# Kernel tuning notes

Hardware: AMD Instinct MI355X
Metric: run time of the kernel (lower is better)

Reference implementation:

```python
import jax, jax.numpy as jnp
import numpy as np

DIM = 512
EPS = 1e-08
N_LAYERS = 3


def setup_inputs() -> dict:
    key = jax.random.key(0)
    ks = jax.random.split(key, 1 + 2 * N_LAYERS)
    B, N1 = 4, 2049  # batch, tokens (1 cls + 2048 feat)
    x = jax.random.normal(ks[0], (B, N1, DIM), dtype=jnp.float32)
    inp = {"x": x}
    s = 1.0 / np.sqrt(DIM)
    for i in range(N_LAYERS):
        inp[f"W{i}"] = jax.random.uniform(ks[1 + 2 * i], (DIM, DIM), jnp.float32, -s, s)
        inp[f"b{i}"] = jax.random.uniform(ks[2 + 2 * i], (DIM,), jnp.float32, -s, s)
    return inp


def _pgcn(x, Ws, bs):
    cls_token = x[:, 0]          # [B, D]
    feat = x[:, 1:]              # [B, N, D]
    n = jnp.linalg.norm(feat, axis=2, keepdims=True)
    feat_norm = feat / jnp.maximum(n, EPS)
    sim = jnp.einsum('bnd,bmd->bnm', feat_norm, feat_norm)  # [B, N, N]
    N = sim.shape[1]
    topk = max(int(N * 0.01), 100)
    # torch.topk(largest=False): kth-smallest value per row is the threshold
    kth_smallest = -jax.lax.top_k(-sim, topk)[0][..., -1:]  # [B, N, 1]
    adj = jnp.where(sim >= kth_smallest, sim, 0.0)
    # 3-layer GCN (skip_connection=False, eval mode -> dropout is identity)
    h = feat
    for W, b in zip(Ws, bs):
        support = jnp.einsum('bnd,de->bne', h, W) + b
        h = jax.nn.relu(jnp.einsum('bnm,bmd->bnd', adj, support))
    return jnp.concatenate([cls_token[:, None, :], h], axis=1)


def reference(x, W0, b0, W1, b1, W2, b2):
    return _pgcn(x, (W0, W1, W2), (b0, b1, b2))
```

## Files before the change

kernel.cpp:

```cpp
#include <hip/hip_runtime.h>
#include <hip/hip_bf16.h>
#include <math.h>

#define DIMV   512
#define NTOK   2048
#define NROWS  2049
#define NB     4
#define KSEL   100
#define EPSV   1e-8f

typedef __bf16 bf16x8 __attribute__((ext_vector_type(8)));
typedef float  f32x4  __attribute__((ext_vector_type(4)));

__device__ __forceinline__ unsigned short f2bf(float f) {
  unsigned int u = __float_as_uint(f);
  u += 0x7fffu + ((u >> 16) & 1u);
  return (unsigned short)(u >> 16);
}
__device__ __forceinline__ float bf2f(unsigned short s) {
  return __uint_as_float(((unsigned int)s) << 16);
}

#define GLDS16(g, l)                                                         \
  __builtin_amdgcn_global_load_lds(                                          \
      (const __attribute__((address_space(1))) void*)(unsigned long long)(g),\
      (__attribute__((address_space(3))) void*)(unsigned int)(unsigned long long)(l), \
      16, 0, 0)

__global__ __launch_bounds__(256) void normalize_kernel(const float* __restrict__ x,
                                                        unsigned short* __restrict__ fhi,
                                                        unsigned short* __restrict__ flo,
                                                        unsigned short* __restrict__ featb) {
  const int wave = blockIdx.x * 4 + (threadIdx.x >> 6);
  const int lane = threadIdx.x & 63;
  const int b = wave / NTOK, r = wave % NTOK;
  const float* src = x + (long)(b * NROWS + 1 + r) * DIMV;
  const long rowoff = (long)(b * NTOK + r) * DIMV;
  float4 v0 = reinterpret_cast<const float4*>(src)[lane];
  float4 v1 = reinterpret_cast<const float4*>(src)[lane + 64];
  ushort4 u0, u1;
  u0.x = f2bf(v0.x); u0.y = f2bf(v0.y); u0.z = f2bf(v0.z); u0.w = f2bf(v0.w);
  u1.x = f2bf(v1.x); u1.y = f2bf(v1.y); u1.z = f2bf(v1.z); u1.w = f2bf(v1.w);
  reinterpret_cast<ushort4*>(featb + rowoff)[lane] = u0;
  reinterpret_cast<ushort4*>(featb + rowoff)[lane + 64] = u1;
  float ss = v0.x*v0.x + v0.y*v0.y + v0.z*v0.z + v0.w*v0.w
           + v1.x*v1.x + v1.y*v1.y + v1.z*v1.z + v1.w*v1.w;
  #pragma unroll
  for (int m = 1; m < 64; m <<= 1) ss += __shfl_xor(ss, m, 64);
  const float scale = 1.0f / fmaxf(sqrtf(ss), EPSV);
  float f[8] = {v0.x*scale, v0.y*scale, v0.z*scale, v0.w*scale,
                v1.x*scale, v1.y*scale, v1.z*scale, v1.w*scale};
  ushort4 h0, h1, l0, l1;
  unsigned short hh[8], ll[8];
  #pragma unroll
  for (int i = 0; i < 8; i++) {
    hh[i] = f2bf(f[i]);
    ll[i] = f2bf(f[i] - bf2f(hh[i]));
  }
  h0.x = hh[0]; h0.y = hh[1]; h0.z = hh[2]; h0.w = hh[3];
  h1.x = hh[4]; h1.y = hh[5]; h1.z = hh[6]; h1.w = hh[7];
  l0.x = ll[0]; l0.y = ll[1]; l0.z = ll[2]; l0.w = ll[3];
  l1.x = ll[4]; l1.y = ll[5]; l1.z = ll[6]; l1.w = ll[7];
  reinterpret_cast<ushort4*>(fhi + rowoff)[lane]      = h0;
  reinterpret_cast<ushort4*>(fhi + rowoff)[lane + 64] = h1;
  reinterpret_cast<ushort4*>(flo + rowoff)[lane]      = l0;
  reinterpret_cast<ushort4*>(flo + rowoff)[lane + 64] = l1;
}

__global__ __launch_bounds__(256) void prep_kernel(const float* __restrict__ W0,
                                                   const float* __restrict__ W1,
                                                   const float* __restrict__ W2,
                                                   unsigned short* __restrict__ WT,
                                                   const float* __restrict__ x,
                                                   float* __restrict__ out) {
  const int z = blockIdx.z;
  if (z == 3) {
    if (blockIdx.y == 0 && blockIdx.x < 8) {
      const int b = blockIdx.x >> 1, half = blockIdx.x & 1;
      const long off = (long)b * NROWS * DIMV + half * 256 + threadIdx.x;
      out[off] = x[off];
    }
    return;
  }
  const float* W = (z == 0) ? W0 : (z == 1) ? W1 : W2;
  unsigned short* WTl = WT + (long)z * DIMV * DIMV;
  __shared__ float tile[32][33];
  const int tx = threadIdx.x & 31, ty = threadIdx.x >> 5;
  const int bx = blockIdx.x, by = blockIdx.y;
  #pragma unroll
  for (int s = 0; s < 32; s += 8)
    tile[ty + s][tx] = W[(long)(by * 32 + ty + s) * DIMV + bx * 32 + tx];
  __syncthreads();
  #pragma unroll
  for (int s = 0; s < 32; s += 8)
    WTl[(long)(bx * 32 + ty + s) * DIMV + by * 32 + tx] = f2bf(tile[tx][ty + s]);
}

__global__ __launch_bounds__(256)
void sim_split_kernel(const unsigned short* __restrict__ Fhi,
                      const unsigned short* __restrict__ Flo,
                      float* __restrict__ C)
{
  __shared__ unsigned short AsH[128 * 32];
  __shared__ unsigned short AsL[128 * 32];
  __shared__ unsigned short BsH[128 * 32];
  __shared__ unsigned short BsL[128 * 32];
  const int t = threadIdx.x;
  const int l = t & 63;
  const int w = t >> 6;
  const int wr = w >> 1, wc = w & 1;
  const int zb = blockIdx.z;
  const int ti = blockIdx.x;
  int by = (int)((sqrtf(8.0f * (float)ti + 1.0f) - 1.0f) * 0.5f);
  while ((by + 1) * (by + 2) / 2 <= ti) by++;
  while (by * (by + 1) / 2 > ti) by--;
  const int bx = ti - by * (by + 1) / 2;
  const unsigned short* Ahi = Fhi + (long)zb * NTOK * DIMV;
  const unsigned short* Alo = Flo + (long)zb * NTOK * DIMV;
  const int row0 = by * 128;
  const int col0 = bx * 128;

  f32x4 acc[4][4];
  #pragma unroll
  for (int m = 0; m < 4; m++)
    #pragma unroll
    for (int n = 0; n < 4; n++) acc[m][n] = (f32x4){0.f, 0.f, 0.f, 0.f};

  const int r0 = t >> 2;
  const int r1 = 64 + (t >> 2);
  const int part = t & 3;
  const size_t base0 = (size_t)((t & 192) * 8);
  const size_t base1 = (size_t)((256 + (t & 192)) * 8);
  const int fr = l & 15, fg = l >> 4;

  for (int k0 = 0; k0 < DIMV; k0 += 32) {
    GLDS16(Ahi + (long)(row0 + r0) * DIMV + k0 + part * 8, AsH + base0);
    GLDS16(Ahi + (long)(row0 + r1) * DIMV + k0 + part * 8, AsH + base1);
    GLDS16(Alo + (long)(row0 + r0) * DIMV + k0 + part * 8, AsL + base0);
    GLDS16(Alo + (long)(row0 + r1) * DIMV + k0 + part * 8, AsL + base1);
    GLDS16(Ahi + (long)(col0 + r0) * DIMV + k0 + part * 8, BsH + base0);
    GLDS16(Ahi + (long)(col0 + r1) * DIMV + k0 + part * 8, BsH + base1);
    GLDS16(Alo + (long)(col0 + r0) * DIMV + k0 + part * 8, BsL + base0);
    GLDS16(Alo + (long)(col0 + r1) * DIMV + k0 + part * 8, BsL + base1);
    __syncthreads();

    bf16x8 ah[4], al[4], bh[4], bl[4];
    #pragma unroll
    for (int m = 0; m < 4; m++) {
      const int off = (wr * 64 + m * 16 + fr) * 32 + fg * 8;
      ah[m] = *reinterpret_cast<const bf16x8*>(&AsH[off]);
      al[m] = *reinterpret_cast<const bf16x8*>(&AsL[off]);
    }
    #pragma unroll
    for (int n = 0; n < 4; n++) {
      const int off = (wc * 64 + n * 16 + fr) * 32 + fg * 8;
      bh[n] = *reinterpret_cast<const bf16x8*>(&BsH[off]);
      bl[n] = *reinterpret_cast<const bf16x8*>(&BsL[off]);
    }
    #pragma unroll
    for (int m = 0; m < 4; m++)
      #pragma unroll
      for (int n = 0; n < 4; n++) {
        acc[m][n] = __builtin_amdgcn_mfma_f32_16x16x32_bf16(ah[m], bh[n], acc[m][n], 0, 0, 0);
        acc[m][n] = __builtin_amdgcn_mfma_f32_16x16x32_bf16(ah[m], bl[n], acc[m][n], 0, 0, 0);
        acc[m][n] = __builtin_amdgcn_mfma_f32_16x16x32_bf16(al[m], bh[n], acc[m][n], 0, 0, 0);
      }
    __syncthreads();
  }

  float* Cb = C + (long)zb * NTOK * NTOK;
  #pragma unroll
  for (int m = 0; m < 4; m++)
    #pragma unroll
    for (int r = 0; r < 4; r++) {
      const int row = row0 + wr * 64 + m * 16 + fg * 4 + r;
      #pragma unroll
      for (int n = 0; n < 4; n++) {
        const int col = col0 + wc * 64 + n * 16 + fr;
        Cb[(long)row * NTOK + col] = acc[m][n][r];
      }
    }
  if (bx != by) {
    #pragma unroll
    for (int m = 0; m < 4; m++)
      #pragma unroll
      for (int r = 0; r < 4; r++) {
        const int row = row0 + wr * 64 + m * 16 + fg * 4 + r;
        #pragma unroll
        for (int n = 0; n < 4; n++) {
          const int col = col0 + wc * 64 + n * 16 + fr;
          Cb[(long)col * NTOK + row] = acc[m][n][r];
        }
      }
  }
}

template<bool BIAS, bool RELU, bool BF16OUT>
__device__ __forceinline__
void gemm_body(const unsigned short* __restrict__ A,
               const unsigned short* __restrict__ Bt,
               const float* __restrict__ bias,
               void* __restrict__ Cv,
               int K, int lda, int ldb, int ldc,
               long sA, long sB, long sC,
               int bx, int by, int bz,
               unsigned short* As, unsigned short* Bs)
{
  const int t = threadIdx.x;
  const int l = t & 63;
  const int w = t >> 6;
  const int wr = w >> 1, wc = w & 1;
  A  += (long)bz * sA;
  Bt += (long)bz * sB;
  const int row0 = by * 128;
  const int col0 = bx * 64;

  f32x4 acc[4][2];
  #pragma unroll
  for (int m = 0; m < 4; m++)
    #pragma unroll
    for (int n = 0; n < 2; n++) acc[m][n] = (f32x4){0.f, 0.f, 0.f, 0.f};

  const int arow0 = t >> 2;
  const int arow1 = (t + 256) >> 2;
  const int apart = t & 3;
  const int brow  = t >> 2, bpart = t & 3;
  unsigned short* ldsA0 = As + (size_t)((t & 192) * 8);
  unsigned short* ldsA1 = As + (size_t)((256 + (t & 192)) * 8);
  unsigned short* ldsB  = Bs + (size_t)((t & 192) * 8);
  const int fr = l & 15, fg = l >> 4;

  const int nk = K >> 5;
  for (int kk = 0; kk < nk; ++kk) {
    const int k0 = kk << 5;
    GLDS16(A  + (long)(row0 + arow0) * lda + k0 + apart * 8, ldsA0);
    GLDS16(A  + (long)(row0 + arow1) * lda + k0 + apart * 8, ldsA1);
    GLDS16(Bt + (long)(col0 + brow)  * ldb + k0 + bpart * 8, ldsB);
    __syncthreads();

    bf16x8 af[4], bfr[2];
    #pragma unroll
    for (int m = 0; m < 4; m++)
      af[m] = *reinterpret_cast<const bf16x8*>(
          &As[(wr * 64 + m * 16 + fr) * 32 + fg * 8]);
    #pragma unroll
    for (int n = 0; n < 2; n++)
      bfr[n] = *reinterpret_cast<const bf16x8*>(
          &Bs[(wc * 32 + n * 16 + fr) * 32 + fg * 8]);
    #pragma unroll
    for (int m = 0; m < 4; m++)
      #pragma unroll
      for (int n = 0; n < 2; n++)
        acc[m][n] = __builtin_amdgcn_mfma_f32_16x16x32_bf16(af[m], bfr[n],
                                                            acc[m][n], 0, 0, 0);
    __syncthreads();
  }

  #pragma unroll
  for (int m = 0; m < 4; m++) {
    #pragma unroll
    for (int r = 0; r < 4; r++) {
      const int row = row0 + wr * 64 + m * 16 + fg * 4 + r;
      float bv = 0.f;
      if (BIAS) bv = bias[row];
      #pragma unroll
      for (int n = 0; n < 2; n++) {
        const int col = col0 + wc * 32 + n * 16 + fr;
        float v = acc[m][n][r] + bv;
        if (RELU) v = fmaxf(v, 0.f);
        if (BF16OUT)
          ((unsigned short*)Cv)[(long)bz * sC + (long)row * ldc + col] = f2bf(v);
        else
          ((float*)Cv)[(long)bz * sC + (long)row * ldc + col] = v;
      }
    }
  }
}

template<bool BIAS, bool RELU, bool BF16OUT>
__global__ __launch_bounds__(256)
void mfma_gemm(const unsigned short* __restrict__ A,
               const unsigned short* __restrict__ Bt,
               const float* __restrict__ bias,
               void* __restrict__ Cv,
               int K, int lda, int ldb, int ldc,
               long sA, long sB, long sC)
{
  __shared__ unsigned short As[128 * 32];
  __shared__ unsigned short Bs[64 * 32];
  const int nx = gridDim.x, ny = gridDim.y;
  int lin = blockIdx.x + nx * (blockIdx.y + ny * blockIdx.z);
  const int nwg = nx * ny * (int)gridDim.z;
  const int chunk = nwg >> 3;
  lin = (lin & 7) * chunk + (lin >> 3);
  const int bx = lin % nx;
  const int tmp = lin / nx;
  const int by = tmp % ny;
  const int bz = tmp / ny;
  gemm_body<BIAS, RELU, BF16OUT>(A, Bt, bias, Cv, K, lda, ldb, ldc,
                                 sA, sB, sC, bx, by, bz, As, Bs);
}

__global__ __launch_bounds__(256)
void kthgemm_kernel(const float* __restrict__ sim,
                    unsigned short* __restrict__ adjb,
                    const unsigned short* __restrict__ WT0,
                    const unsigned short* __restrict__ hb,
                    const float* __restrict__ bias0,
                    unsigned short* __restrict__ supT)
{
  __shared__ unsigned short As[128 * 32];
  __shared__ unsigned short Bs[64 * 32];
  if (blockIdx.x >= 2048) {
    const int bid = blockIdx.x - 2048;
    const int bx = bid & 31, by = (bid >> 5) & 3, bz = bid >> 7;
    gemm_body<true, false, true>(WT0, hb, bias0, supT,
                                 DIMV, DIMV, DIMV, NTOK,
                                 0L, (long)NTOK * DIMV, (long)DIMV * NTOK,
                                 bx, by, bz, As, Bs);
    return;
  }
  const int wid = blockIdx.x * 4 + (threadIdx.x >> 6);
  const int lane = threadIdx.x & 63;
  const float4* row = reinterpret_cast<const float4*>(sim + (long)wid * NTOK);
  unsigned int key[32];
  #pragma unroll
  for (int i = 0; i < 8; i++) {
    const float4 v = row[lane + i * 64];
    const float f[4] = {v.x, v.y, v.z, v.w};
    #pragma unroll
    for (int j = 0; j < 4; j++) {
      const unsigned int b = __float_as_uint(f[j]);
      key[i * 4 + j] = (b & 0x80000000u) ? ~b : (b | 0x80000000u);
    }
  }
  unsigned int lo = 0u, hi = 0xFFFFFFFFu;
  for (int it = 0; it < 32; ++it) {
    const unsigned int mid =
        (unsigned int)(((unsigned long long)lo + (unsigned long long)hi) >> 1);
    unsigned int total = 0;
    #pragma unroll
    for (int j = 0; j < 32; j++)
      total += (unsigned int)__popcll(__ballot(key[j] <= mid));
    if (total >= KSEL) hi = mid; else lo = mid + 1u;
  }
  ushort4* orow = reinterpret_cast<ushort4*>(adjb + (long)wid * NTOK);
  #pragma unroll
  for (int i = 0; i < 8; i++) {
    ushort4 o;
    unsigned short* op = &o.x;
    #pragma unroll
    for (int j = 0; j < 4; j++) {
      const unsigned int k = key[i * 4 + j];
      const unsigned int bits = (k & 0x80000000u) ? (k ^ 0x80000000u) : ~k;
      op[j] = (k >= lo) ? f2bf(__uint_as_float(bits)) : (unsigned short)0;
    }
    orow[lane + i * 64] = o;
  }
}

extern "C" void kernel_launch(void* const* d_in, const int* in_sizes, int n_in,
                              void* d_out, int out_size, void* d_ws, size_t ws_size,
                              hipStream_t stream) {
  const float* x  = (const float*)d_in[0];
  const float* Ws[3] = {(const float*)d_in[1], (const float*)d_in[3], (const float*)d_in[5]};
  const float* bs[3] = {(const float*)d_in[2], (const float*)d_in[4], (const float*)d_in[6]};
  float* out = (float*)d_out;

  char* ws = (char*)d_ws;
  unsigned short* fhi    = (unsigned short*)(ws);
  unsigned short* flo    = (unsigned short*)(ws + 8388608UL);
  float*          sim    = (float*)(ws + 16777216UL);
  unsigned short* adjb   = (unsigned short*)(ws + 83886080UL);
  unsigned short* supT   = (unsigned short*)(ws + 117440512UL);
  unsigned short* hb     = (unsigned short*)(ws + 125829120UL);
  unsigned short* wtb    = (unsigned short*)(ws + 134217728UL);

  normalize_kernel<<<dim3(NB * NTOK / 4), 256, 0, stream>>>(x, fhi, flo, hb);

  prep_kernel<<<dim3(16, 16, 4), 256, 0, stream>>>(Ws[0], Ws[1], Ws[2], wtb, x, out);

  sim_split_kernel<<<dim3(136, 1, NB), 256, 0, stream>>>(fhi, flo, sim);

  kthgemm_kernel<<<dim3(2560), 256, 0, stream>>>(sim, adjb, wtb, hb, bs[0], supT);

  for (int lyr = 0; lyr < 3; lyr++) {
    if (lyr > 0) {
      mfma_gemm<true, false, true>
          <<<dim3(NTOK/64, DIMV/128, NB), 256, 0, stream>>>(
          wtb + (long)lyr * DIMV * DIMV, hb, bs[lyr], supT,
          DIMV, DIMV, DIMV, NTOK,
          0L, (long)NTOK * DIMV, (long)DIMV * NTOK);
    }
    if (lyr < 2) {
      mfma_gemm<false, true, true>
          <<<dim3(DIMV/64, NTOK/128, NB), 256, 0, stream>>>(
          adjb, supT, nullptr, hb,
          NTOK, NTOK, NTOK, DIMV,
          (long)NTOK * NTOK, (long)DIMV * NTOK, (long)NTOK * DIMV);
    } else {
      mfma_gemm<false, true, false>
          <<<dim3(DIMV/64, NTOK/128, NB), 256, 0, stream>>>(
          adjb, supT, nullptr, out + DIMV,
          NTOK, NTOK, NTOK, DIMV,
          (long)NTOK * NTOK, (long)DIMV * NTOK, (long)NROWS * DIMV);
    }
  }
}
```

Before: 244.6 us.

## Fuse normalize and prep launches, narrow sim tiles, tighten k-th search bounds

```diff
diff --git a/kernel.cpp b/kernel.cpp
--- a/kernel.cpp
+++ b/kernel.cpp
@@ -27,73 +27,75 @@
       (__attribute__((address_space(3))) void*)(unsigned int)(unsigned long long)(l), \
       16, 0, 0)
 
-__global__ __launch_bounds__(256) void normalize_kernel(const float* __restrict__ x,
-                                                        unsigned short* __restrict__ fhi,
-                                                        unsigned short* __restrict__ flo,
-                                                        unsigned short* __restrict__ featb) {
-  const int wave = blockIdx.x * 4 + (threadIdx.x >> 6);
-  const int lane = threadIdx.x & 63;
-  const int b = wave / NTOK, r = wave % NTOK;
-  const float* src = x + (long)(b * NROWS + 1 + r) * DIMV;
-  const long rowoff = (long)(b * NTOK + r) * DIMV;
-  float4 v0 = reinterpret_cast<const float4*>(src)[lane];
-  float4 v1 = reinterpret_cast<const float4*>(src)[lane + 64];
-  ushort4 u0, u1;
-  u0.x = f2bf(v0.x); u0.y = f2bf(v0.y); u0.z = f2bf(v0.z); u0.w = f2bf(v0.w);
-  u1.x = f2bf(v1.x); u1.y = f2bf(v1.y); u1.z = f2bf(v1.z); u1.w = f2bf(v1.w);
-  reinterpret_cast<ushort4*>(featb + rowoff)[lane] = u0;
-  reinterpret_cast<ushort4*>(featb + rowoff)[lane + 64] = u1;
-  float ss = v0.x*v0.x + v0.y*v0.y + v0.z*v0.z + v0.w*v0.w
-           + v1.x*v1.x + v1.y*v1.y + v1.z*v1.z + v1.w*v1.w;
-  #pragma unroll
-  for (int m = 1; m < 64; m <<= 1) ss += __shfl_xor(ss, m, 64);
-  const float scale = 1.0f / fmaxf(sqrtf(ss), EPSV);
-  float f[8] = {v0.x*scale, v0.y*scale, v0.z*scale, v0.w*scale,
-                v1.x*scale, v1.y*scale, v1.z*scale, v1.w*scale};
-  ushort4 h0, h1, l0, l1;
-  unsigned short hh[8], ll[8];
-  #pragma unroll
-  for (int i = 0; i < 8; i++) {
-    hh[i] = f2bf(f[i]);
-    ll[i] = f2bf(f[i] - bf2f(hh[i]));
-  }
-  h0.x = hh[0]; h0.y = hh[1]; h0.z = hh[2]; h0.w = hh[3];
-  h1.x = hh[4]; h1.y = hh[5]; h1.z = hh[6]; h1.w = hh[7];
-  l0.x = ll[0]; l0.y = ll[1]; l0.z = ll[2]; l0.w = ll[3];
-  l1.x = ll[4]; l1.y = ll[5]; l1.z = ll[6]; l1.w = ll[7];
-  reinterpret_cast<ushort4*>(fhi + rowoff)[lane]      = h0;
-  reinterpret_cast<ushort4*>(fhi + rowoff)[lane + 64] = h1;
-  reinterpret_cast<ushort4*>(flo + rowoff)[lane]      = l0;
-  reinterpret_cast<ushort4*>(flo + rowoff)[lane + 64] = l1;
-}
-
-__global__ __launch_bounds__(256) void prep_kernel(const float* __restrict__ W0,
-                                                   const float* __restrict__ W1,
-                                                   const float* __restrict__ W2,
-                                                   unsigned short* __restrict__ WT,
-                                                   const float* __restrict__ x,
-                                                   float* __restrict__ out) {
-  const int z = blockIdx.z;
-  if (z == 3) {
-    if (blockIdx.y == 0 && blockIdx.x < 8) {
-      const int b = blockIdx.x >> 1, half = blockIdx.x & 1;
-      const long off = (long)b * NROWS * DIMV + half * 256 + threadIdx.x;
-      out[off] = x[off];
-    }
-    return;
-  }
-  const float* W = (z == 0) ? W0 : (z == 1) ? W1 : W2;
-  unsigned short* WTl = WT + (long)z * DIMV * DIMV;
+__global__ __launch_bounds__(256)
+void normprep_kernel(const float* __restrict__ x,
+                     unsigned short* __restrict__ fhi,
+                     unsigned short* __restrict__ flo,
+                     unsigned short* __restrict__ featb,
+                     const float* __restrict__ W0,
+                     const float* __restrict__ W1,
+                     const float* __restrict__ W2,
+                     unsigned short* __restrict__ WT,
+                     float* __restrict__ out)
+{
   __shared__ float tile[32][33];
-  const int tx = threadIdx.x & 31, ty = threadIdx.x >> 5;
-  const int bx = blockIdx.x, by = blockIdx.y;
-  #pragma unroll
-  for (int s = 0; s < 32; s += 8)
-    tile[ty + s][tx] = W[(long)(by * 32 + ty + s) * DIMV + bx * 32 + tx];
-  __syncthreads();
-  #pragma unroll
-  for (int s = 0; s < 32; s += 8)
-    WTl[(long)(bx * 32 + ty + s) * DIMV + by * 32 + tx] = f2bf(tile[tx][ty + s]);
+  const int bid = blockIdx.x;
+  if (bid < 2048) {
+    const int wave = bid * 4 + (threadIdx.x >> 6);
+    const int lane = threadIdx.x & 63;
+    const int b = wave / NTOK, r = wave % NTOK;
+    const float* src = x + (long)(b * NROWS + 1 + r) * DIMV;
+    const long rowoff = (long)(b * NTOK + r) * DIMV;
+    float4 v0 = reinterpret_cast<const float4*>(src)[lane];
+    float4 v1 = reinterpret_cast<const float4*>(src)[lane + 64];
+    ushort4 u0, u1;
+    u0.x = f2bf(v0.x); u0.y = f2bf(v0.y); u0.z = f2bf(v0.z); u0.w = f2bf(v0.w);
+    u1.x = f2bf(v1.x); u1.y = f2bf(v1.y); u1.z = f2bf(v1.z); u1.w = f2bf(v1.w);
+    reinterpret_cast<ushort4*>(featb + rowoff)[lane] = u0;
+    reinterpret_cast<ushort4*>(featb + rowoff)[lane + 64] = u1;
+    float ss = v0.x*v0.x + v0.y*v0.y + v0.z*v0.z + v0.w*v0.w
+             + v1.x*v1.x + v1.y*v1.y + v1.z*v1.z + v1.w*v1.w;
+    #pragma unroll
+    for (int m = 1; m < 64; m <<= 1) ss += __shfl_xor(ss, m, 64);
+    const float scale = 1.0f / fmaxf(sqrtf(ss), EPSV);
+    float f[8] = {v0.x*scale, v0.y*scale, v0.z*scale, v0.w*scale,
+                  v1.x*scale, v1.y*scale, v1.z*scale, v1.w*scale};
+    ushort4 h0, h1, l0, l1;
+    unsigned short hh[8], ll[8];
+    #pragma unroll
+    for (int i = 0; i < 8; i++) {
+      hh[i] = f2bf(f[i]);
+      ll[i] = f2bf(f[i] - bf2f(hh[i]));
+    }
+    h0.x = hh[0]; h0.y = hh[1]; h0.z = hh[2]; h0.w = hh[3];
+    h1.x = hh[4]; h1.y = hh[5]; h1.z = hh[6]; h1.w = hh[7];
+    l0.x = ll[0]; l0.y = ll[1]; l0.z = ll[2]; l0.w = ll[3];
+    l1.x = ll[4]; l1.y = ll[5]; l1.z = ll[6]; l1.w = ll[7];
+    reinterpret_cast<ushort4*>(fhi + rowoff)[lane]      = h0;
+    reinterpret_cast<ushort4*>(fhi + rowoff)[lane + 64] = h1;
+    reinterpret_cast<ushort4*>(flo + rowoff)[lane]      = l0;
+    reinterpret_cast<ushort4*>(flo + rowoff)[lane + 64] = l1;
+  } else if (bid < 2816) {
+    const int idx = bid - 2048;
+    const int z = idx >> 8;
+    const int t2 = idx & 255;
+    const int bx = t2 & 15, by = t2 >> 4;
+    const float* W = (z == 0) ? W0 : (z == 1) ? W1 : W2;
+    unsigned short* WTl = WT + (long)z * DIMV * DIMV;
+    const int tx = threadIdx.x & 31, ty = threadIdx.x >> 5;
+    #pragma unroll
+    for (int s = 0; s < 32; s += 8)
+      tile[ty + s][tx] = W[(long)(by * 32 + ty + s) * DIMV + bx * 32 + tx];
+    __syncthreads();
+    #pragma unroll
+    for (int s = 0; s < 32; s += 8)
+      WTl[(long)(bx * 32 + ty + s) * DIMV + by * 32 + tx] = f2bf(tile[tx][ty + s]);
+  } else {
+    const int cb = bid - 2816;
+    const int b = cb >> 1, half = cb & 1;
+    const long off = (long)b * NROWS * DIMV + half * 256 + threadIdx.x;
+    out[off] = x[off];
+  }
 }
 
 __global__ __launch_bounds__(256)
@@ -103,48 +105,48 @@
 {
   __shared__ unsigned short AsH[128 * 32];
   __shared__ unsigned short AsL[128 * 32];
-  __shared__ unsigned short BsH[128 * 32];
-  __shared__ unsigned short BsL[128 * 32];
+  __shared__ unsigned short BsH[64 * 32];
+  __shared__ unsigned short BsL[64 * 32];
   const int t = threadIdx.x;
   const int l = t & 63;
   const int w = t >> 6;
   const int wr = w >> 1, wc = w & 1;
   const int zb = blockIdx.z;
   const int ti = blockIdx.x;
-  int by = (int)((sqrtf(8.0f * (float)ti + 1.0f) - 1.0f) * 0.5f);
-  while ((by + 1) * (by + 2) / 2 <= ti) by++;
-  while (by * (by + 1) / 2 > ti) by--;
-  const int bx = ti - by * (by + 1) / 2;
+  int by = (int)((sqrtf(4.0f * (float)ti + 1.0f) - 1.0f) * 0.5f);
+  while ((by + 1) * (by + 2) <= ti) by++;
+  while (by * (by + 1) > ti) by--;
+  const int bx = ti - by * (by + 1);
   const unsigned short* Ahi = Fhi + (long)zb * NTOK * DIMV;
   const unsigned short* Alo = Flo + (long)zb * NTOK * DIMV;
   const int row0 = by * 128;
-  const int col0 = bx * 128;
-
-  f32x4 acc[4][4];
+  const int col0 = bx * 64;
+
+  f32x4 acc[4][2];
   #pragma unroll
   for (int m = 0; m < 4; m++)
     #pragma unroll
-    for (int n = 0; n < 4; n++) acc[m][n] = (f32x4){0.f, 0.f, 0.f, 0.f};
-
-  const int r0 = t >> 2;
-  const int r1 = 64 + (t >> 2);
-  const int part = t & 3;
-  const size_t base0 = (size_t)((t & 192) * 8);
-  const size_t base1 = (size_t)((256 + (t & 192)) * 8);
+    for (int n = 0; n < 2; n++) acc[m][n] = (f32x4){0.f, 0.f, 0.f, 0.f};
+
+  const int arow0 = t >> 2;
+  const int arow1 = (t + 256) >> 2;
+  const int apart = t & 3;
+  const int brow  = t >> 2, bpart = t & 3;
+  const size_t baseA0 = (size_t)((t & 192) * 8);
+  const size_t baseA1 = (size_t)((256 + (t & 192)) * 8);
+  const size_t baseB  = (size_t)((t & 192) * 8);
   const int fr = l & 15, fg = l >> 4;
 
   for (int k0 = 0; k0 < DIMV; k0 += 32) {
-    GLDS16(Ahi + (long)(row0 + r0) * DIMV + k0 + part * 8, AsH + base0);
-    GLDS16(Ahi + (long)(row0 + r1) * DIMV + k0 + part * 8, AsH + base1);
-    GLDS16(Alo + (long)(row0 + r0) * DIMV + k0 + part * 8, AsL + base0);
-    GLDS16(Alo + (long)(row0 + r1) * DIMV + k0 + part * 8, AsL + base1);
-    GLDS16(Ahi + (long)(col0 + r0) * DIMV + k0 + part * 8, BsH + base0);
-    GLDS16(Ahi + (long)(col0 + r1) * DIMV + k0 + part * 8, BsH + base1);
-    GLDS16(Alo + (long)(col0 + r0) * DIMV + k0 + part * 8, BsL + base0);
-    GLDS16(Alo + (long)(col0 + r1) * DIMV + k0 + part * 8, BsL + base1);
-    __syncthreads();
-
-    bf16x8 ah[4], al[4], bh[4], bl[4];
+    GLDS16(Ahi + (long)(row0 + arow0) * DIMV + k0 + apart * 8, AsH + baseA0);
+    GLDS16(Ahi + (long)(row0 + arow1) * DIMV + k0 + apart * 8, AsH + baseA1);
+    GLDS16(Alo + (long)(row0 + arow0) * DIMV + k0 + apart * 8, AsL + baseA0);
+    GLDS16(Alo + (long)(row0 + arow1) * DIMV + k0 + apart * 8, AsL + baseA1);
+    GLDS16(Ahi + (long)(col0 + brow)  * DIMV + k0 + bpart * 8, BsH + baseB);
+    GLDS16(Alo + (long)(col0 + brow)  * DIMV + k0 + bpart * 8, BsL + baseB);
+    __syncthreads();
+
+    bf16x8 ah[4], al[4], bh[2], bl[2];
     #pragma unroll
     for (int m = 0; m < 4; m++) {
       const int off = (wr * 64 + m * 16 + fr) * 32 + fg * 8;
@@ -152,15 +154,15 @@
       al[m] = *reinterpret_cast<const bf16x8*>(&AsL[off]);
     }
     #pragma unroll
-    for (int n = 0; n < 4; n++) {
-      const int off = (wc * 64 + n * 16 + fr) * 32 + fg * 8;
+    for (int n = 0; n < 2; n++) {
+      const int off = (wc * 32 + n * 16 + fr) * 32 + fg * 8;
       bh[n] = *reinterpret_cast<const bf16x8*>(&BsH[off]);
       bl[n] = *reinterpret_cast<const bf16x8*>(&BsL[off]);
     }
     #pragma unroll
     for (int m = 0; m < 4; m++)
       #pragma unroll
-      for (int n = 0; n < 4; n++) {
+      for (int n = 0; n < 2; n++) {
         acc[m][n] = __builtin_amdgcn_mfma_f32_16x16x32_bf16(ah[m], bh[n], acc[m][n], 0, 0, 0);
         acc[m][n] = __builtin_amdgcn_mfma_f32_16x16x32_bf16(ah[m], bl[n], acc[m][n], 0, 0, 0);
         acc[m][n] = __builtin_amdgcn_mfma_f32_16x16x32_bf16(al[m], bh[n], acc[m][n], 0, 0, 0);
@@ -175,24 +177,12 @@
     for (int r = 0; r < 4; r++) {
       const int row = row0 + wr * 64 + m * 16 + fg * 4 + r;
       #pragma unroll
-      for (int n = 0; n < 4; n++) {
-        const int col = col0 + wc * 64 + n * 16 + fr;
+      for (int n = 0; n < 2; n++) {
+        const int col = col0 + wc * 32 + n * 16 + fr;
         Cb[(long)row * NTOK + col] = acc[m][n][r];
+        Cb[(long)col * NTOK + row] = acc[m][n][r];
       }
     }
-  if (bx != by) {
-    #pragma unroll
-    for (int m = 0; m < 4; m++)
-      #pragma unroll
-      for (int r = 0; r < 4; r++) {
-        const int row = row0 + wr * 64 + m * 16 + fg * 4 + r;
-        #pragma unroll
-        for (int n = 0; n < 4; n++) {
-          const int col = col0 + wc * 64 + n * 16 + fr;
-          Cb[(long)col * NTOK + row] = acc[m][n][r];
-        }
-      }
-  }
 }
 
 template<bool BIAS, bool RELU, bool BF16OUT>
@@ -311,8 +301,8 @@
 {
   __shared__ unsigned short As[128 * 32];
   __shared__ unsigned short Bs[64 * 32];
-  if (blockIdx.x >= 2048) {
-    const int bid = blockIdx.x - 2048;
+  if (blockIdx.x < 512) {
+    const int bid = blockIdx.x;
     const int bx = bid & 31, by = (bid >> 5) & 3, bz = bid >> 7;
     gemm_body<true, false, true>(WT0, hb, bias0, supT,
                                  DIMV, DIMV, DIMV, NTOK,
@@ -320,7 +310,7 @@
                                  bx, by, bz, As, Bs);
     return;
   }
-  const int wid = blockIdx.x * 4 + (threadIdx.x >> 6);
+  const int wid = (blockIdx.x - 512) * 4 + (threadIdx.x >> 6);
   const int lane = threadIdx.x & 63;
   const float4* row = reinterpret_cast<const float4*>(sim + (long)wid * NTOK);
   unsigned int key[32];
@@ -334,8 +324,8 @@
       key[i * 4 + j] = (b & 0x80000000u) ? ~b : (b | 0x80000000u);
     }
   }
-  unsigned int lo = 0u, hi = 0xFFFFFFFFu;
-  for (int it = 0; it < 32; ++it) {
+  unsigned int lo = 0x406FFFFFu, hi = 0xBF900000u;
+  for (int it = 0; it < 31; ++it) {
     const unsigned int mid =
         (unsigned int)(((unsigned long long)lo + (unsigned long long)hi) >> 1);
     unsigned int total = 0;
@@ -376,11 +366,10 @@
   unsigned short* hb     = (unsigned short*)(ws + 125829120UL);
   unsigned short* wtb    = (unsigned short*)(ws + 134217728UL);
 
-  normalize_kernel<<<dim3(NB * NTOK / 4), 256, 0, stream>>>(x, fhi, flo, hb);
-
-  prep_kernel<<<dim3(16, 16, 4), 256, 0, stream>>>(Ws[0], Ws[1], Ws[2], wtb, x, out);
-
-  sim_split_kernel<<<dim3(136, 1, NB), 256, 0, stream>>>(fhi, flo, sim);
+  normprep_kernel<<<dim3(2824), 256, 0, stream>>>(
+      x, fhi, flo, hb, Ws[0], Ws[1], Ws[2], wtb, out);
+
+  sim_split_kernel<<<dim3(272, 1, NB), 256, 0, stream>>>(fhi, flo, sim);
 
   kthgemm_kernel<<<dim3(2560), 256, 0, stream>>>(sim, adjb, wtb, hb, bs[0], supT);
 
```

Measured after the change: 257.7 us. 1.05x slower.
